# Kernel optimization log

Measured on AMD Instinct MI355X. Metric: run time of the kernel, lower is better.

Reference implementation:

```python
import jax, jax.numpy as jnp
import numpy as np

FP8_MAX = 448.0  # torch.finfo(torch.float8_e4m3fn).max
FP8_MIN = -448.0


def per_tensor_quantize(t):
    # amax = max(|min|, |max|) over the whole tensor
    amax = jnp.maximum(jnp.abs(jnp.min(t)), jnp.abs(jnp.max(t)))
    scale = FP8_MAX / jnp.clip(amax, 1e-12, None)
    q = jnp.clip(t * scale, FP8_MIN, FP8_MAX).astype(jnp.float8_e4m3fn)
    inv_scale = (1.0 / scale).astype(jnp.float32)
    return q, inv_scale


def setup_inputs() -> dict:
    key = jax.random.key(0)
    k1, k2 = jax.random.split(key)
    B, S, D_IN, D_OUT = 8, 8192, 1024, 1024
    x = jax.random.normal(k1, (B, S, D_IN), dtype=jnp.float32)
    w = jax.random.normal(k2, (D_OUT, D_IN), dtype=jnp.float32) * 0.02
    qweight, weight_scale = per_tensor_quantize(w)  # fp8 weight + scalar fp32 scale
    return {"x": x, "qweight": qweight, "weight_scale": weight_scale}


def reference(x, qweight, weight_scale):
    # dynamic per-tensor activation quantization (quantize -> fp8)
    qinput, act_scale = per_tensor_quantize(x)
    # fp8 gemm with inline dequant scales (manual dequant-linear path, bias=None)
    A = qinput.astype(x.dtype) * act_scale          # [B, S, D_in]
    W = qweight.astype(x.dtype) * weight_scale.astype(x.dtype)  # [D_out, D_in]
    out = jnp.einsum('bsk,nk->bsn', A, W)           # [B, S, D_out]
    return out
```

## Files before the change

kernel.cpp:

```cpp
#include <hip/hip_runtime.h>
#include <hip/hip_fp8.h>
#include <stdint.h>
#include <cmath>

using f32x4 = __attribute__((ext_vector_type(4))) float;
using i32x4 = __attribute__((ext_vector_type(4))) int;
using i32x8 = __attribute__((ext_vector_type(8))) int;

#define FP8MAX 448.0f

__device__ __forceinline__ void gload_lds16(const void* g, void* l) {
  __builtin_amdgcn_global_load_lds(
      (const __attribute__((address_space(1))) unsigned int*)g,
      (__attribute__((address_space(3))) unsigned int*)l,
      16, 0, 0);
}

__device__ __forceinline__ uint8_t to_fp8(float v) {
  __hip_fp8_e4m3 q(fminf(fmaxf(v, -FP8MAX), FP8MAX));
  return q.__x;
}

__global__ void wconv(const uint8_t* __restrict__ w, uint8_t* __restrict__ q,
                      unsigned int* __restrict__ amax_u, int n) {
  if (blockIdx.x == 0 && threadIdx.x == 0) amax_u[0] = 0u;

  const float* wf = (const float*)w;
  const unsigned short* wh = (const unsigned short*)w;
  int f32ok = 1, bf16ok = 1;
  for (int i = threadIdx.x; i < 4096; i += 256) {
    float v = wf[i];
    if (!(isfinite(v) && fabsf(v) <= FP8MAX)) f32ok = 0;
    else { __hip_fp8_e4m3 qq(v); if ((float)qq != v) f32ok = 0; }
    float hv = __uint_as_float(((unsigned int)wh[i]) << 16);
    if (!(isfinite(hv) && fabsf(hv) <= FP8MAX)) bf16ok = 0;
    else { __hip_fp8_e4m3 qh(hv); if ((float)qh != hv) bf16ok = 0; }
  }
  __shared__ int sf, sb;
  if (threadIdx.x == 0) { sf = 1; sb = 1; }
  __syncthreads();
  if (!f32ok) atomicAnd(&sf, 0);
  if (!bf16ok) atomicAnd(&sb, 0);
  __syncthreads();
  unsigned int f = sf ? 2u : (sb ? 1u : 0u);

  int i0 = (blockIdx.x * blockDim.x + threadIdx.x) * 4;
  if (i0 >= n) return;
  uint32_t out;
  if (f == 2) {
    float4 v = *(const float4*)((const float*)w + i0);
    out = (uint32_t)to_fp8(v.x) | ((uint32_t)to_fp8(v.y) << 8) |
          ((uint32_t)to_fp8(v.z) << 16) | ((uint32_t)to_fp8(v.w) << 24);
  } else if (f == 1) {
    ushort4 h = *(const ushort4*)((const unsigned short*)w + i0);
    float a = __uint_as_float(((unsigned int)h.x) << 16);
    float b = __uint_as_float(((unsigned int)h.y) << 16);
    float c = __uint_as_float(((unsigned int)h.z) << 16);
    float d = __uint_as_float(((unsigned int)h.w) << 16);
    out = (uint32_t)to_fp8(a) | ((uint32_t)to_fp8(b) << 8) |
          ((uint32_t)to_fp8(c) << 16) | ((uint32_t)to_fp8(d) << 24);
  } else {
    out = *(const uint32_t*)(w + i0);
  }
  *(uint32_t*)(q + i0) = out;
}

__global__ void amax_kernel(const float* __restrict__ x, size_t n4,
                            unsigned int* __restrict__ amax_u) {
  const float4* x4 = (const float4*)x;
  float m = 0.0f;
  size_t stride = (size_t)gridDim.x * blockDim.x;
  for (size_t i = (size_t)blockIdx.x * blockDim.x + threadIdx.x; i < n4; i += stride) {
    float4 v = x4[i];
    m = fmaxf(m, fmaxf(fmaxf(fabsf(v.x), fabsf(v.y)),
                       fmaxf(fabsf(v.z), fabsf(v.w))));
  }
  #pragma unroll
  for (int off = 32; off > 0; off >>= 1)
    m = fmaxf(m, __shfl_xor(m, off));
  __shared__ float sm[16];
  int wid = threadIdx.x >> 6;
  if ((threadIdx.x & 63) == 0) sm[wid] = m;
  __syncthreads();
  if (threadIdx.x == 0) {
    int nw = blockDim.x >> 6;
    float r = sm[0];
    for (int i = 1; i < nw; i++) r = fmaxf(r, sm[i]);
    atomicMax(amax_u, __float_as_uint(r));
  }
}

__global__ void quant_kernel(const float* __restrict__ x,
                             uint8_t* __restrict__ q,
                             const float* __restrict__ amax_p, size_t n16) {
  float amax = fmaxf(amax_p[0], 1e-12f);
  float scale = FP8MAX / amax;
  const float4* x4 = (const float4*)x;
  uint4* q16 = (uint4*)q;
  size_t stride = (size_t)gridDim.x * blockDim.x;
  for (size_t i = (size_t)blockIdx.x * blockDim.x + threadIdx.x; i < n16; i += stride) {
    uint32_t w[4];
    #pragma unroll
    for (int j = 0; j < 4; j++) {
      float4 v = x4[i * 4 + j];
      w[j] = (uint32_t)to_fp8(v.x * scale) | ((uint32_t)to_fp8(v.y * scale) << 8) |
             ((uint32_t)to_fp8(v.z * scale) << 16) | ((uint32_t)to_fp8(v.w * scale) << 24);
    }
    uint4 o; o.x = w[0]; o.y = w[1]; o.z = w[2]; o.w = w[3];
    q16[i] = o;
  }
}

#define BM 128
#define BN 128
#define BK 128

__global__ __launch_bounds__(256) void gemm_fp8(
    const uint8_t* __restrict__ A,
    const uint8_t* __restrict__ B,
    float* __restrict__ C,
    const float* __restrict__ amax_p,
    const float* __restrict__ wscale_p,
    int M, int N, int K) {
  __shared__ uint8_t lds_a[2][BM * BK];
  __shared__ uint8_t lds_b[2][BN * BK];

  int nwg = gridDim.x;
  int cpx = nwg >> 3;
  int swz = (blockIdx.x & 7) * cpx + (blockIdx.x >> 3);

  int nstrips = N / BN;
  int bm = (swz / nstrips) * BM;
  int bn = (swz % nstrips) * BN;

  int t = threadIdx.x;
  int lane = t & 63;
  int wave = t >> 6;
  int wm = (wave >> 1) * 64;
  int wn = (wave & 1) * 64;

  float amax = fmaxf(amax_p[0], 1e-12f);
  float scale = FP8MAX / amax;
  float s = (1.0f / scale) * wscale_p[0];

  f32x4 acc[4][4] = {};

  const int rt = t >> 3;
  const int ct = t & 7;
  const int stoff = wave * 1024;

  const int lr = lane & 15;
  const int x7 = lr & 7;
  const int g2 = (lane >> 4) << 1;
  const int c0 = ((g2 ^ x7) << 4);
  const int c1 = (((g2 + 1) ^ x7) << 4);
  int abase[4], bbase[4];
  #pragma unroll
  for (int i = 0; i < 4; i++) abase[i] = (wm + i * 16 + lr) * BK;
  #pragma unroll
  for (int j = 0; j < 4; j++) bbase[j] = (wn + j * 16 + lr) * BK;

  auto stage = [&](uint8_t* dstA, uint8_t* dstB, int k0) {
    #pragma unroll
    for (int p = 0; p < 4; ++p) {
      int r = p * 32 + rt;
      int gc = (ct ^ (r & 7)) * 16;
      gload_lds16(A + (size_t)(bm + r) * K + k0 + gc, dstA + stoff + p * 4096);
      gload_lds16(B + (size_t)(bn + r) * K + k0 + gc, dstB + stoff + p * 4096);
    }
  };

  auto compute = [&](const uint8_t* baseA, const uint8_t* baseB) {
    i32x8 af[4], bf[4];
    #pragma unroll
    for (int i = 0; i < 4; i++) {
      i32x4 lo = *(const i32x4*)(baseA + abase[i] + c0);
      i32x4 hi = *(const i32x4*)(baseA + abase[i] + c1);
      af[i] = (i32x8){lo.x, lo.y, lo.z, lo.w, hi.x, hi.y, hi.z, hi.w};
    }
    #pragma unroll
    for (int j = 0; j < 4; j++) {
      i32x4 lo = *(const i32x4*)(baseB + bbase[j] + c0);
      i32x4 hi = *(const i32x4*)(baseB + bbase[j] + c1);
      bf[j] = (i32x8){lo.x, lo.y, lo.z, lo.w, hi.x, hi.y, hi.z, hi.w};
    }
    #pragma unroll
    for (int i = 0; i < 4; i++)
      #pragma unroll
      for (int j = 0; j < 4; j++)
        acc[i][j] = __builtin_amdgcn_mfma_scale_f32_16x16x128_f8f6f4(
            af[i], bf[j], acc[i][j],
            0 , 0 ,
            0, 0x7f7f7f7f,
            0, 0x7f7f7f7f);
  };

  const int KITERS = K / BK;
  stage(lds_a[0], lds_b[0], 0);
  __syncthreads();

  for (int it = 0; it < KITERS; it += 2) {
    if (it + 1 < KITERS) stage(lds_a[1], lds_b[1], (it + 1) * BK);
    compute(lds_a[0], lds_b[0]);
    __syncthreads();
    if (it + 2 < KITERS) stage(lds_a[0], lds_b[0], (it + 2) * BK);
    compute(lds_a[1], lds_b[1]);
    __syncthreads();
  }

  #pragma unroll
  for (int i = 0; i < 4; i++) {
    #pragma unroll
    for (int j = 0; j < 4; j++) {
      int row = bm + wm + i * 16 + (lane >> 4) * 4;
      int col = bn + wn + j * 16 + (lane & 15);
      #pragma unroll
      for (int r = 0; r < 4; r++)
        C[(size_t)(row + r) * N + col] = acc[i][j][r] * s;
    }
  }
}

extern "C" void kernel_launch(void* const* d_in, const int* in_sizes, int n_in,
                              void* d_out, int out_size, void* d_ws, size_t ws_size,
                              hipStream_t stream) {
  const float* x = (const float*)d_in[0];
  const uint8_t* wraw = (const uint8_t*)d_in[1];
  const float* wscale = (const float*)d_in[2];
  float* out = (float*)d_out;

  long long in0 = in_sizes[0];
  long long in1 = in_sizes[1];
  double kd = sqrt((double)in0 * (double)in1 / (double)out_size);
  long long K = (long long)(kd + 0.5);
  long long M = in0 / K;
  long long N = in1 / K;

  unsigned int* amax_u = (unsigned int*)d_ws;
  const float* amax_f = (const float*)d_ws;
  uint8_t* qw = (uint8_t*)d_ws + 4096;
  uint8_t* qx = (uint8_t*)d_ws + (2u << 20);

  wconv<<<(unsigned)(in1 / 4 / 256), 256, 0, stream>>>(wraw, qw, amax_u, (int)in1);
  amax_kernel<<<2048, 256, 0, stream>>>(x, (size_t)(in0 / 4), amax_u);
  quant_kernel<<<2048, 256, 0, stream>>>(x, qx, amax_f, (size_t)(in0 / 16));

  dim3 grid((unsigned)((M / BM) * (N / BN)));
  gemm_fp8<<<grid, 256, 0, stream>>>(qx, qw, out, amax_f, wscale,
                                     (int)M, (int)N, (int)K);
}
```

Measured before the change: 283.2 us.

## Use 512-thread GEMM blocks with finer waitcnt pipelining and MFMA priority

The FP8 GEMM now runs 8 waves per 128x128 tile, each owning a 32x64 sub-tile, which halves accumulator registers per wave and targets higher occupancy. The double-buffered loop is rewritten to issue the next stage and then wait with explicit vmcnt counts and raw s_barriers instead of __syncthreads. MFMA blocks are raised in scheduling priority with s_setprio. B fragments are now reloaded from LDS by more waves, which adds LDS read traffic, and the hand-written waitcnt values depend on the exact number of loads issued per stage.

Result: faster. 270.8 us (-4.4%).

```diff
diff --git a/kernel.cpp b/kernel.cpp
--- a/kernel.cpp
+++ b/kernel.cpp
@@ -115,15 +115,14 @@
 #define BN 128
 #define BK 128
 
-__global__ __launch_bounds__(256) void gemm_fp8(
+__global__ __launch_bounds__(512, 4) void gemm_fp8(
     const uint8_t* __restrict__ A,
     const uint8_t* __restrict__ B,
     float* __restrict__ C,
     const float* __restrict__ amax_p,
     const float* __restrict__ wscale_p,
     int M, int N, int K) {
-  __shared__ uint8_t lds_a[2][BM * BK];
-  __shared__ uint8_t lds_b[2][BN * BK];
+  __shared__ uint8_t lds[2][2][BM * BK];
 
   int nwg = gridDim.x;
   int cpx = nwg >> 3;
@@ -136,44 +135,46 @@
   int t = threadIdx.x;
   int lane = t & 63;
   int wave = t >> 6;
-  int wm = (wave >> 1) * 64;
+  int wm = (wave >> 1) * 32;
   int wn = (wave & 1) * 64;
 
   float amax = fmaxf(amax_p[0], 1e-12f);
   float scale = FP8MAX / amax;
   float s = (1.0f / scale) * wscale_p[0];
 
-  f32x4 acc[4][4] = {};
+  f32x4 acc[2][4] = {};
 
   const int rt = t >> 3;
   const int ct = t & 7;
-  const int stoff = wave * 1024;
 
   const int lr = lane & 15;
   const int x7 = lr & 7;
   const int g2 = (lane >> 4) << 1;
   const int c0 = ((g2 ^ x7) << 4);
   const int c1 = (((g2 + 1) ^ x7) << 4);
-  int abase[4], bbase[4];
-  #pragma unroll
-  for (int i = 0; i < 4; i++) abase[i] = (wm + i * 16 + lr) * BK;
+  int abase[2], bbase[4];
+  #pragma unroll
+  for (int i = 0; i < 2; i++) abase[i] = (wm + i * 16 + lr) * BK;
   #pragma unroll
   for (int j = 0; j < 4; j++) bbase[j] = (wn + j * 16 + lr) * BK;
 
-  auto stage = [&](uint8_t* dstA, uint8_t* dstB, int k0) {
-    #pragma unroll
-    for (int p = 0; p < 4; ++p) {
-      int r = p * 32 + rt;
+  auto stage = [&](int buf, int kt) {
+    int k0 = kt * BK;
+    #pragma unroll
+    for (int p = 0; p < 2; ++p) {
+      int r = p * 64 + rt;
       int gc = (ct ^ (r & 7)) * 16;
-      gload_lds16(A + (size_t)(bm + r) * K + k0 + gc, dstA + stoff + p * 4096);
-      gload_lds16(B + (size_t)(bn + r) * K + k0 + gc, dstB + stoff + p * 4096);
+      gload_lds16(A + (size_t)(bm + r) * K + k0 + gc, &lds[buf][0][p * 8192 + t * 16]);
+      gload_lds16(B + (size_t)(bn + r) * K + k0 + gc, &lds[buf][1][p * 8192 + t * 16]);
     }
   };
 
-  auto compute = [&](const uint8_t* baseA, const uint8_t* baseB) {
-    i32x8 af[4], bf[4];
-    #pragma unroll
-    for (int i = 0; i < 4; i++) {
+  auto compute = [&](int buf) {
+    const uint8_t* baseA = &lds[buf][0][0];
+    const uint8_t* baseB = &lds[buf][1][0];
+    i32x8 af[2], bf[4];
+    #pragma unroll
+    for (int i = 0; i < 2; i++) {
       i32x4 lo = *(const i32x4*)(baseA + abase[i] + c0);
       i32x4 hi = *(const i32x4*)(baseA + abase[i] + c1);
       af[i] = (i32x8){lo.x, lo.y, lo.z, lo.w, hi.x, hi.y, hi.z, hi.w};
@@ -184,32 +185,38 @@
       i32x4 hi = *(const i32x4*)(baseB + bbase[j] + c1);
       bf[j] = (i32x8){lo.x, lo.y, lo.z, lo.w, hi.x, hi.y, hi.z, hi.w};
     }
-    #pragma unroll
-    for (int i = 0; i < 4; i++)
+    __builtin_amdgcn_s_setprio(1);
+    #pragma unroll
+    for (int j = 0; j < 4; j++)
       #pragma unroll
-      for (int j = 0; j < 4; j++)
+      for (int i = 0; i < 2; i++)
         acc[i][j] = __builtin_amdgcn_mfma_scale_f32_16x16x128_f8f6f4(
             af[i], bf[j], acc[i][j],
             0 , 0 ,
             0, 0x7f7f7f7f,
             0, 0x7f7f7f7f);
+    __builtin_amdgcn_s_setprio(0);
   };
 
   const int KITERS = K / BK;
-  stage(lds_a[0], lds_b[0], 0);
-  __syncthreads();
-
-  for (int it = 0; it < KITERS; it += 2) {
-    if (it + 1 < KITERS) stage(lds_a[1], lds_b[1], (it + 1) * BK);
-    compute(lds_a[0], lds_b[0]);
-    __syncthreads();
-    if (it + 2 < KITERS) stage(lds_a[0], lds_b[0], (it + 2) * BK);
-    compute(lds_a[1], lds_b[1]);
-    __syncthreads();
-  }
-
-  #pragma unroll
-  for (int i = 0; i < 4; i++) {
+  stage(0, 0);
+
+  for (int it = 0; it < KITERS; ++it) {
+    int cur = it & 1;
+    if (it + 1 < KITERS) {
+      stage(cur ^ 1, it + 1);
+      asm volatile("s_waitcnt vmcnt(4)" ::: "memory");
+    } else {
+      asm volatile("s_waitcnt vmcnt(0)" ::: "memory");
+    }
+    __builtin_amdgcn_s_barrier();
+    __builtin_amdgcn_sched_barrier(0);
+    compute(cur);
+    __builtin_amdgcn_s_barrier();
+  }
+
+  #pragma unroll
+  for (int i = 0; i < 2; i++) {
     #pragma unroll
     for (int j = 0; j < 4; j++) {
       int row = bm + wm + i * 16 + (lane >> 4) * 4;
@@ -246,6 +253,6 @@
   quant_kernel<<<2048, 256, 0, stream>>>(x, qx, amax_f, (size_t)(in0 / 16));
 
   dim3 grid((unsigned)((M / BM) * (N / BN)));
-  gemm_fp8<<<grid, 256, 0, stream>>>(qx, qw, out, amax_f, wscale,
+  gemm_fp8<<<grid, 512, 0, stream>>>(qx, qw, out, amax_f, wscale,
                                      (int)M, (int)N, (int)K);
 }
```
